# Kernel tuning notes

Hardware: AMD Instinct MI355X
Metric: run time of the kernel (lower is better)

The kernel has to match this reference:

```python
import jax, jax.numpy as jnp
import numpy as np

EPS = 1e-12  # torch F.normalize eps
NUM_HEADS = 4
DT = 0.25
NUM_STEPS = 4


def _l2norm(x, axis=-1):
    n = jnp.sqrt(jnp.sum(x * x, axis=axis, keepdims=True))
    return x / jnp.maximum(n, EPS)


def setup_inputs() -> dict:
    key = jax.random.key(0)
    k0, k1, k2, k3, k4 = jax.random.split(key, 5)
    B, T, D = 4, 2048, 256
    z = jax.random.normal(k0, (B, T, D), dtype=jnp.float32)
    omega = jax.random.normal(k1, (1, 1, D), dtype=jnp.float32) * 0.1
    Wqk = jax.random.normal(k2, (2 * D, D), dtype=jnp.float32) * (1.0 / np.sqrt(D))
    Wout = jax.random.normal(k3, (D, D), dtype=jnp.float32) * (1.0 / np.sqrt(D))
    bout = jax.random.normal(k4, (D,), dtype=jnp.float32) * 0.01
    return {"z": z, "omega": omega, "Wqk": Wqk, "Wout": Wout, "bout": bout}


def _kuramoto(x, omega, Wqk, Wout, bout):
    # x: [B, T, D]
    B, T, D = x.shape
    hd = D // NUM_HEADS
    qk = x @ Wqk.T  # [B, T, 2D]
    q, k = jnp.split(qk, 2, axis=-1)
    q = _l2norm(q.reshape(B, T, NUM_HEADS, hd))  # cosine-normalized per head
    k = _l2norm(k.reshape(B, T, NUM_HEADS, hd))
    # coupling: [B, H, T, T] cosine similarity
    coupling = jnp.einsum("bqhd,bkhd->bhqk", q, k)
    # sin nonlinearity replaces softmax
    force = jnp.einsum("bhqk,bkhd->bqhd", jnp.sin(coupling), k).reshape(B, T, D)
    return omega + force @ Wout.T + bout


def reference(z, omega, Wqk, Wout, bout):
    def f(x):
        return _kuramoto(x, omega, Wqk, Wout, bout)

    x = z
    for _ in range(NUM_STEPS):
        x = _l2norm(x)
        k1 = f(x)
        k2 = f(x + DT / 2 * k1)
        k3 = f(x + DT / 2 * k2)
        k4 = f(x + DT * k3)
        x = x + DT / 6 * (k1 + 2 * k2 + 2 * k3 + k4)
    return _l2norm(x)
```

## Files before the change

kernel.cpp:

```cpp
#include <hip/hip_runtime.h>
#include <cmath>

#define NB 4
#define TT 2048
#define DD 256
#define NH 4
#define BT (NB*TT)

static constexpr float DT_ = 0.25f;

typedef _Float16 f16x8 __attribute__((ext_vector_type(8)));
typedef _Float16 f16x4 __attribute__((ext_vector_type(4)));
typedef float    f32x4 __attribute__((ext_vector_type(4)));

static constexpr size_t HSZ = (size_t)NB * NH * TT * 64;
static constexpr size_t FSZ = (size_t)BT * 256;

__device__ __forceinline__ void gload16(const void* g, void* l) {
    __builtin_amdgcn_global_load_lds(
        (const __attribute__((address_space(1))) void*)g,
        (__attribute__((address_space(3))) void*)l,
        16, 0, 0);
}

__global__ __launch_bounds__(256)
void split_weights(const float* __restrict__ Wqk, const float* __restrict__ Wout,
                   _Float16* __restrict__ WqkH, _Float16* __restrict__ WqkL,
                   _Float16* __restrict__ WoutH, _Float16* __restrict__ WoutL)
{
    const int idx = blockIdx.x * 256 + threadIdx.x;
    const float4 v = (idx < 32768) ? ((const float4*)Wqk)[idx]
                                   : ((const float4*)Wout)[idx - 32768];
    f16x4 h, l;
    h[0]=(_Float16)v.x; l[0]=(_Float16)(v.x-(float)h[0]);
    h[1]=(_Float16)v.y; l[1]=(_Float16)(v.y-(float)h[1]);
    h[2]=(_Float16)v.z; l[2]=(_Float16)(v.z-(float)h[2]);
    h[3]=(_Float16)v.w; l[3]=(_Float16)(v.w-(float)h[3]);
    if (idx < 32768) { ((f16x4*)WqkH)[idx] = h; ((f16x4*)WqkL)[idx] = l; }
    else { ((f16x4*)WoutH)[idx-32768] = h; ((f16x4*)WoutL)[idx-32768] = l; }
}

__global__ __launch_bounds__(256)
void comb_weights(const float* __restrict__ Wqk, const float* __restrict__ Wout,
                  const float* __restrict__ omega, const float* __restrict__ bout,
                  _Float16* __restrict__ WcombH, _Float16* __restrict__ WcombL,
                  float* __restrict__ qkob)
{
    __shared__ float qrow[256];
    __shared__ float pr[256];
    const int n = blockIdx.x;
    const int k = threadIdx.x;
    qrow[k] = Wqk[n * 256 + k];
    __syncthreads();
    float s = 0.f;
    for (int m = 0; m < 256; ++m) s = fmaf(qrow[m], Wout[m * 256 + k], s);
    const _Float16 h = (_Float16)s;
    WcombH[n * 256 + k] = h;
    WcombL[n * 256 + k] = (_Float16)(s - (float)h);
    pr[k] = (omega[k] + bout[k]) * qrow[k];
    __syncthreads();
    if (k == 0) {
        float t = 0.f;
        for (int i = 0; i < 256; ++i) t += pr[i];
        qkob[n] = t;
    }
}

__global__ __launch_bounds__(256)
void l2norm_rows(const float* __restrict__ src, float* __restrict__ dst,
                 _Float16* __restrict__ dstH, _Float16* __restrict__ dstL) {
    const int wave = threadIdx.x >> 6;
    const int lane = threadIdx.x & 63;
    const size_t row = (size_t)blockIdx.x * 4 + wave;
    float4 v = ((const float4*)(src + row * DD))[lane];
    float ss = v.x*v.x + v.y*v.y + v.z*v.z + v.w*v.w;
    #pragma unroll
    for (int off = 32; off; off >>= 1) ss += __shfl_xor(ss, off, 64);
    const float inv = 1.0f / fmaxf(sqrtf(ss), 1e-12f);
    v.x *= inv; v.y *= inv; v.z *= inv; v.w *= inv;
    ((float4*)(dst + row * DD))[lane] = v;
    if (dstH != nullptr) {
        f16x4 h, l;
        h[0]=(_Float16)v.x; l[0]=(_Float16)(v.x-(float)h[0]);
        h[1]=(_Float16)v.y; l[1]=(_Float16)(v.y-(float)h[1]);
        h[2]=(_Float16)v.z; l[2]=(_Float16)(v.z-(float)h[2]);
        h[3]=(_Float16)v.w; l[3]=(_Float16)(v.w-(float)h[3]);
        ((f16x4*)(dstH + row * DD))[lane] = h;
        ((f16x4*)(dstL + row * DD))[lane] = l;
    }
}

__global__ __launch_bounds__(256)
void reduce_F(const float* __restrict__ Fp, float* __restrict__ Facc,
              _Float16* __restrict__ SH, _Float16* __restrict__ SL, int faccm)
{
    const size_t idx = (size_t)blockIdx.x * 256 + threadIdx.x;
    const float4 a = ((const float4*)Fp)[idx];
    const float4 b = ((const float4*)(Fp + FSZ))[idx];
    const float4 c = ((const float4*)(Fp + 2*FSZ))[idx];
    float4 s = make_float4(a.x+b.x+c.x, a.y+b.y+c.y, a.z+b.z+c.z, a.w+b.w+c.w);
    if (faccm == 1) {
        ((float4*)Facc)[idx] = s;
    } else if (faccm == 2) {
        float4 f = ((const float4*)Facc)[idx];
        f.x += 2.f*s.x; f.y += 2.f*s.y; f.z += 2.f*s.z; f.w += 2.f*s.w;
        ((float4*)Facc)[idx] = f;
    } else {
        const float4 f = ((const float4*)Facc)[idx];
        s.x += f.x; s.y += f.y; s.z += f.z; s.w += f.w;
    }
    f16x4 h, l;
    h[0]=(_Float16)s.x; l[0]=(_Float16)(s.x-(float)h[0]);
    h[1]=(_Float16)s.y; l[1]=(_Float16)(s.y-(float)h[1]);
    h[2]=(_Float16)s.z; l[2]=(_Float16)(s.z-(float)h[2]);
    h[3]=(_Float16)s.w; l[3]=(_Float16)(s.w-(float)h[3]);
    ((f16x4*)SH)[idx] = h;
    ((f16x4*)SL)[idx] = l;
}

__global__ __launch_bounds__(256, 3)
void gemm_mfma(const _Float16* __restrict__ AH, const _Float16* __restrict__ AL,
               const _Float16* __restrict__ BH, const _Float16* __restrict__ BL,
               float* __restrict__ qkx, const float* __restrict__ qkob,
               const float* __restrict__ omega, const float* __restrict__ bout,
               const float* __restrict__ xin, float* __restrict__ xout,
               _Float16* __restrict__ Qhi, _Float16* __restrict__ Qlo,
               _Float16* __restrict__ Khi, _Float16* __restrict__ Klo,
               _Float16* __restrict__ KtrH,
               int mode, float cc)
{
    __shared__ _Float16 Ah[128 * 64];
    __shared__ _Float16 Al[128 * 64];
    __shared__ _Float16 Bh[64 * 64];
    __shared__ _Float16 Bl[64 * 64];
    const int m0 = blockIdx.x * 128, n0 = blockIdx.y * 64;
    const int t  = threadIdx.x;
    const int w  = t >> 6;
    const int l  = t & 63;
    const int lr = l & 15;
    const int lq = l >> 4;
    const int m7 = lr & 7;
    const int rr = l >> 3;
    const int cg = ((l & 7) ^ rr) * 8;

    f32x4 acc[2][4];
    #pragma unroll
    for (int s = 0; s < 2; ++s)
        #pragma unroll
        for (int nt = 0; nt < 4; ++nt) acc[s][nt] = (f32x4){0.f,0.f,0.f,0.f};

    for (int kc = 0; kc < 4; ++kc) {
        const int k0 = kc * 64;
        __syncthreads();
        #pragma unroll
        for (int a = 0; a < 4; ++a) {
            const int rg = 8*w + 32*a;
            gload16(AH + (size_t)(m0 + rg + rr) * 256 + k0 + cg, &Ah[rg * 64]);
            gload16(AL + (size_t)(m0 + rg + rr) * 256 + k0 + cg, &Al[rg * 64]);
            if (a < 2) {
                gload16(BH + (size_t)(n0 + rg + rr) * 256 + k0 + cg, &Bh[rg * 64]);
                gload16(BL + (size_t)(n0 + rg + rr) * 256 + k0 + cg, &Bl[rg * 64]);
            }
        }
        __syncthreads();
        #pragma unroll
        for (int c = 0; c < 2; ++c) {
            const int xo = (((4*c + lq) ^ m7) << 4);
            f16x8 ah[2], al[2], bh[4], bl[4];
            #pragma unroll
            for (int s = 0; s < 2; ++s) {
                ah[s] = *(const f16x8*)((const char*)Ah + (32*w + 16*s + lr) * 128 + xo);
                al[s] = *(const f16x8*)((const char*)Al + (32*w + 16*s + lr) * 128 + xo);
            }
            #pragma unroll
            for (int nt = 0; nt < 4; ++nt) {
                bh[nt] = *(const f16x8*)((const char*)Bh + (16*nt + lr) * 128 + xo);
                bl[nt] = *(const f16x8*)((const char*)Bl + (16*nt + lr) * 128 + xo);
            }
            #pragma unroll
            for (int s = 0; s < 2; ++s)
                #pragma unroll
                for (int nt = 0; nt < 4; ++nt) {
                    acc[s][nt] = __builtin_amdgcn_mfma_f32_16x16x32_f16(ah[s], bh[nt], acc[s][nt], 0, 0, 0);
                    acc[s][nt] = __builtin_amdgcn_mfma_f32_16x16x32_f16(ah[s], bl[nt], acc[s][nt], 0, 0, 0);
                    acc[s][nt] = __builtin_amdgcn_mfma_f32_16x16x32_f16(al[s], bh[nt], acc[s][nt], 0, 0, 0);
                }
        }
    }

    if (mode == 2) {
        #pragma unroll
        for (int s = 0; s < 2; ++s) {
            const int row0 = m0 + 32*w + 16*s + 4*lq;
            #pragma unroll
            for (int nt = 0; nt < 4; ++nt) {
                const int col = n0 + 16*nt + lr;
                const float ob = omega[col] + bout[col];
                #pragma unroll
                for (int r = 0; r < 4; ++r) {
                    const size_t off = (size_t)(row0 + r) * 256 + col;
                    xout[off] = xin[off] + (DT_ / 6.0f) * acc[s][nt][r] + DT_ * ob;
                }
            }
        }
    } else {
        float val[2][4][4];
        #pragma unroll
        for (int s = 0; s < 2; ++s) {
            const int row0 = m0 + 32*w + 16*s + 4*lq;
            #pragma unroll
            for (int nt = 0; nt < 4; ++nt) {
                const int col = n0 + 16*nt + lr;
                #pragma unroll
                for (int r = 0; r < 4; ++r) {
                    const size_t qo = (size_t)(row0 + r) * 512 + col;
                    if (mode == 0) {
                        val[s][nt][r] = acc[s][nt][r];
                        qkx[qo] = acc[s][nt][r];
                    } else {
                        val[s][nt][r] = qkx[qo] + cc * (acc[s][nt][r] + qkob[col]);
                    }
                }
            }
        }
        float ss[2][4];
        #pragma unroll
        for (int s = 0; s < 2; ++s)
            #pragma unroll
            for (int r = 0; r < 4; ++r) {
                float v = 0.f;
                #pragma unroll
                for (int nt = 0; nt < 4; ++nt) v += val[s][nt][r] * val[s][nt][r];
                ss[s][r] = v;
            }
        #pragma unroll
        for (int off = 1; off < 16; off <<= 1)
            #pragma unroll
            for (int s = 0; s < 2; ++s)
                #pragma unroll
                for (int r = 0; r < 4; ++r)
                    ss[s][r] += __shfl_xor(ss[s][r], off, 64);
        const int  b    = m0 >> 11;
        const int  h    = (n0 >> 6) & 3;
        const bool is_k = (n0 >= 256);
        const size_t bhi = (size_t)b * NH + h;
        _Float16* dhi = (is_k ? Khi : Qhi) + bhi * (size_t)TT * 64;
        _Float16* dlo = (is_k ? Klo : Qlo) + bhi * (size_t)TT * 64;
        const int mloc = m0 & (TT - 1);
        #pragma unroll
        for (int s = 0; s < 2; ++s) {
            const int r0 = 32*w + 16*s + 4*lq;
            float inv[4];
            #pragma unroll
            for (int r = 0; r < 4; ++r) inv[r] = 1.0f / fmaxf(sqrtf(ss[s][r]), 1e-12f);
            #pragma unroll
            for (int nt = 0; nt < 4; ++nt) {
                const int d = 16*nt + lr;
                f16x4 hv, lv;
                #pragma unroll
                for (int r = 0; r < 4; ++r) {
                    const float v2 = val[s][nt][r] * inv[r];
                    hv[r] = (_Float16)v2;
                    lv[r] = (_Float16)(v2 - (float)hv[r]);
                    dhi[(size_t)(mloc + r0 + r) * 64 + d] = hv[r];
                    dlo[(size_t)(mloc + r0 + r) * 64 + d] = lv[r];
                }
                if (is_k) {
                    const size_t tb = bhi * (size_t)64 * TT + (size_t)d * TT + mloc + r0;
                    *(f16x4*)(KtrH + tb) = hv;
                }
            }
        }
    }
}

__global__ __launch_bounds__(256, 3)
void kuramoto_attn(const _Float16* __restrict__ Qhi, const _Float16* __restrict__ Qlo,
                   const _Float16* __restrict__ Khi, const _Float16* __restrict__ Klo,
                   const _Float16* __restrict__ KtrH,
                   float* __restrict__ Fp)
{
    __shared__ _Float16 KjH[64 * 64];
    __shared__ _Float16 KjL[64 * 64];
    __shared__ _Float16 KdH[64 * 64];
    __shared__ _Float16 Pw[4][2][16 * 64];
    const int bh = blockIdx.x;
    const int b  = bh >> 2, h = bh & 3;
    const size_t base  = (size_t)bh * TT * 64;
    const size_t tbase = (size_t)bh * 64 * TT;
    const int t0 = blockIdx.y * 11;
    const int tn = (blockIdx.y == 2) ? 10 : 11;
    float* Fout = Fp + (size_t)blockIdx.y * FSZ;
    const int t = threadIdx.x;
    const int w = t >> 6;
    const int l = t & 63;
    const int lr = l & 15;
    const int lq = l >> 4;
    const int i0 = blockIdx.z * 128 + w * 32;
    const int m7 = lr & 7;
    const int x0 = ((lq ^ m7) << 4);
    const int x1 = (((lq + 4) ^ m7) << 4);
    const int rr = l >> 3;
    const int lc8 = (l & 7) * 8;
    const int sw = ((l & 7) ^ rr) * 8;
    const int rg = 8 * w + rr;

    f16x8 qh[2][2], ql[2][2];
    #pragma unroll
    for (int s = 0; s < 2; ++s) {
        const size_t qoff = base + (size_t)(i0 + 16*s + lr) * 64 + lq * 8;
        qh[s][0] = *(const f16x8*)(Qhi + qoff);
        qh[s][1] = *(const f16x8*)(Qhi + qoff + 32);
        ql[s][0] = *(const f16x8*)(Qlo + qoff);
        ql[s][1] = *(const f16x8*)(Qlo + qoff + 32);
    }

    f32x4 Facc[2][4];
    #pragma unroll
    for (int s = 0; s < 2; ++s)
        #pragma unroll
        for (int nt = 0; nt < 4; ++nt) Facc[s][nt] = (f32x4){0.f, 0.f, 0.f, 0.f};

    uint4 gA0, gA1, gB0, gB1, gC0, gC1;
#define GLOAD(TTi) do { \
        const int j0_ = (t0 + (TTi)) * 64; \
        gA0 = *(const uint4*)(Khi  + base  + (size_t)(j0_ + rg)      * 64 + lc8); \
        gA1 = *(const uint4*)(Khi  + base  + (size_t)(j0_ + rg + 32) * 64 + lc8); \
        gB0 = *(const uint4*)(Klo  + base  + (size_t)(j0_ + rg)      * 64 + lc8); \
        gB1 = *(const uint4*)(Klo  + base  + (size_t)(j0_ + rg + 32) * 64 + lc8); \
        gC0 = *(const uint4*)(KtrH + tbase + (size_t)rg        * TT + j0_ + lc8); \
        gC1 = *(const uint4*)(KtrH + tbase + (size_t)(rg + 32) * TT + j0_ + lc8); \
    } while (0)

    GLOAD(0);

    for (int tt = 0; tt < tn; ++tt) {
        *(uint4*)&KjH[rg * 64 + sw]        = gA0;
        *(uint4*)&KjH[(rg + 32) * 64 + sw] = gA1;
        *(uint4*)&KjL[rg * 64 + sw]        = gB0;
        *(uint4*)&KjL[(rg + 32) * 64 + sw] = gB1;
        *(uint4*)&KdH[rg * 64 + sw]        = gC0;
        *(uint4*)&KdH[(rg + 32) * 64 + sw] = gC1;
        if (tt + 1 < tn) GLOAD(tt + 1);
        asm volatile("s_waitcnt lgkmcnt(0)" ::: "memory");
        __builtin_amdgcn_s_barrier();
        asm volatile("" ::: "memory");

        #pragma unroll
        for (int nt = 0; nt < 4; ++nt) {
            const int rb = (16*nt + lr) * 128;
            f16x8 kh0 = *(const f16x8*)((const char*)KjH + rb + x0);
            f16x8 kh1 = *(const f16x8*)((const char*)KjH + rb + x1);
            f16x8 kl0 = *(const f16x8*)((const char*)KjL + rb + x0);
            f16x8 kl1 = *(const f16x8*)((const char*)KjL + rb + x1);
            #pragma unroll
            for (int s = 0; s < 2; ++s) {
                f32x4 a = (f32x4){0.f, 0.f, 0.f, 0.f};
                __builtin_amdgcn_s_setprio(1);
                a = __builtin_amdgcn_mfma_f32_16x16x32_f16(kh0, qh[s][0], a, 0, 0, 0);
                a = __builtin_amdgcn_mfma_f32_16x16x32_f16(kh1, qh[s][1], a, 0, 0, 0);
                a = __builtin_amdgcn_mfma_f32_16x16x32_f16(kl0, qh[s][0], a, 0, 0, 0);
                a = __builtin_amdgcn_mfma_f32_16x16x32_f16(kl1, qh[s][1], a, 0, 0, 0);
                a = __builtin_amdgcn_mfma_f32_16x16x32_f16(kh0, ql[s][0], a, 0, 0, 0);
                a = __builtin_amdgcn_mfma_f32_16x16x32_f16(kh1, ql[s][1], a, 0, 0, 0);
                __builtin_amdgcn_s_setprio(0);
                f16x4 pv;
                #pragma unroll
                for (int r = 0; r < 4; ++r) pv[r] = (_Float16)__sinf(a[r]);
                *(f16x4*)((char*)&Pw[w][0][0] + ((int)sizeof(_Float16))*0 + s * 2048 + lr * 128
                          + (((2*nt + (lq >> 1)) ^ m7) << 4) + ((lq & 1) << 3)) = pv;
            }
        }
        f16x8 ph[2][2];
        #pragma unroll
        for (int s = 0; s < 2; ++s) {
            ph[s][0] = *(const f16x8*)((const char*)&Pw[w][0][0] + s * 2048 + lr * 128 + x0);
            ph[s][1] = *(const f16x8*)((const char*)&Pw[w][0][0] + s * 2048 + lr * 128 + x1);
        }
        #pragma unroll
        for (int nt = 0; nt < 4; ++nt) {
            const int rb = (16*nt + lr) * 128;
            f16x8 kh0 = *(const f16x8*)((const char*)KdH + rb + x0);
            f16x8 kh1 = *(const f16x8*)((const char*)KdH + rb + x1);
            __builtin_amdgcn_s_setprio(1);
            #pragma unroll
            for (int s = 0; s < 2; ++s) {
                Facc[s][nt] = __builtin_amdgcn_mfma_f32_16x16x32_f16(ph[s][0], kh0, Facc[s][nt], 0, 0, 0);
                Facc[s][nt] = __builtin_amdgcn_mfma_f32_16x16x32_f16(ph[s][1], kh1, Facc[s][nt], 0, 0, 0);
            }
            __builtin_amdgcn_s_setprio(0);
        }
        __builtin_amdgcn_s_barrier();
        asm volatile("" ::: "memory");
    }
#undef GLOAD

    #pragma unroll
    for (int s = 0; s < 2; ++s) {
        float* fo = Fout + ((size_t)b * TT + i0 + 16*s + 4*lq) * 256 + h * 64 + lr;
        #pragma unroll
        for (int nt = 0; nt < 4; ++nt)
            #pragma unroll
            for (int r = 0; r < 4; ++r)
                fo[(size_t)r * 256 + nt * 16] = Facc[s][nt][r];
    }
}

extern "C" void kernel_launch(void* const* d_in, const int* in_sizes, int n_in,
                              void* d_out, int out_size, void* d_ws, size_t ws_size,
                              hipStream_t stream) {
    const float* z     = (const float*)d_in[0];
    const float* omega = (const float*)d_in[1];
    const float* Wqk   = (const float*)d_in[2];
    const float* Wout  = (const float*)d_in[3];
    const float* bout  = (const float*)d_in[4];

    float* x    = (float*)d_ws;
    float* Facc = x + FSZ;
    float* Fp   = Facc + FSZ;
    float* qkx  = Fp + 3 * FSZ;
    float* qkob = qkx + (size_t)BT * 512;
    _Float16* xsH  = (_Float16*)(qkob + 512);
    _Float16* xsL  = xsH  + FSZ;
    _Float16* Qhi  = xsL  + FSZ;
    _Float16* Qlo  = Qhi  + HSZ;
    _Float16* Khi  = Qlo  + HSZ;
    _Float16* Klo  = Khi  + HSZ;
    _Float16* KtrH = Klo  + HSZ;
    _Float16* WqkH = KtrH + HSZ;
    _Float16* WqkL = WqkH + (size_t)512 * 256;
    _Float16* WoutH= WqkL + (size_t)512 * 256;
    _Float16* WoutL= WoutH + (size_t)256 * 256;
    _Float16* WcombH = WoutL + (size_t)256 * 256;
    _Float16* WcombL = WcombH + (size_t)512 * 256;

    split_weights<<<192, 256, 0, stream>>>(Wqk, Wout, WqkH, WqkL, WoutH, WoutL);
    comb_weights<<<512, 256, 0, stream>>>(Wqk, Wout, omega, bout, WcombH, WcombL, qkob);

    for (int step = 0; step < 4; ++step) {
        l2norm_rows<<<BT / 4, 256, 0, stream>>>(step == 0 ? z : x, x, xsH, xsL);
        gemm_mfma<<<dim3(BT / 128, 8), 256, 0, stream>>>(
            xsH, xsL, WqkH, WqkL, qkx, nullptr,
            nullptr, nullptr, nullptr, nullptr,
            Qhi, Qlo, Khi, Klo, KtrH, 0, 0.f);
        kuramoto_attn<<<dim3(NB * NH, 3, TT / 128), 256, 0, stream>>>(
            Qhi, Qlo, Khi, Klo, KtrH, Fp);
        for (int s = 1; s <= 3; ++s) {
            const float cs = (s == 3) ? 0.25f : 0.125f;
            reduce_F<<<2048, 256, 0, stream>>>(Fp, Facc, xsH, xsL, (s == 1) ? 1 : 2);
            gemm_mfma<<<dim3(BT / 128, 8), 256, 0, stream>>>(
                xsH, xsL, WcombH, WcombL, qkx, qkob,
                nullptr, nullptr, nullptr, nullptr,
                Qhi, Qlo, Khi, Klo, KtrH, 1, cs);
            kuramoto_attn<<<dim3(NB * NH, 3, TT / 128), 256, 0, stream>>>(
                Qhi, Qlo, Khi, Klo, KtrH, Fp);
        }
        reduce_F<<<2048, 256, 0, stream>>>(Fp, Facc, xsH, xsL, 3);
        gemm_mfma<<<dim3(BT / 128, 4), 256, 0, stream>>>(
            xsH, xsL, WoutH, WoutL, nullptr, nullptr,
            omega, bout, x, x,
            nullptr, nullptr, nullptr, nullptr, nullptr, 2, 0.f);
    }
    l2norm_rows<<<BT / 4, 256, 0, stream>>>(x, (float*)d_out, nullptr, nullptr);
}
```

Baseline: 1.161 ms.

## Prefetch next K-chunk in GEMM and stage transposed K through LDS

The GEMM main loop now loads all fragments of a chunk into registers, then issues the global-to-LDS loads for the next chunk before running the MFMAs, so memory traffic overlaps with compute. Launch bounds drop from 3 to 2 waves per SIMD to allow the extra fragment registers. The transposed K output is first written to a swizzled LDS tile and then stored with coalesced 16-byte global writes instead of scattered 8-byte writes. The trade-off is lower occupancy and an extra barrier in the K epilogue.

Result: no change. 1.153 ms, median of 2 (-0.6%).

```diff
diff --git a/kernel.cpp b/kernel.cpp
--- a/kernel.cpp
+++ b/kernel.cpp
@@ -118,7 +118,7 @@
     ((f16x4*)SL)[idx] = l;
 }
 
-__global__ __launch_bounds__(256, 3)
+__global__ __launch_bounds__(256, 2)
 void gemm_mfma(const _Float16* __restrict__ AH, const _Float16* __restrict__ AL,
                const _Float16* __restrict__ BH, const _Float16* __restrict__ BL,
                float* __restrict__ qkx, const float* __restrict__ qkob,
@@ -149,44 +149,57 @@
         #pragma unroll
         for (int nt = 0; nt < 4; ++nt) acc[s][nt] = (f32x4){0.f,0.f,0.f,0.f};
 
+#define GSTAGE(K0) do { \
+        _Pragma("unroll") \
+        for (int a = 0; a < 4; ++a) { \
+            const int rg = 8*w + 32*a; \
+            gload16(AH + (size_t)(m0 + rg + rr) * 256 + (K0) + cg, &Ah[rg * 64]); \
+            gload16(AL + (size_t)(m0 + rg + rr) * 256 + (K0) + cg, &Al[rg * 64]); \
+            if (a < 2) { \
+                gload16(BH + (size_t)(n0 + rg + rr) * 256 + (K0) + cg, &Bh[rg * 64]); \
+                gload16(BL + (size_t)(n0 + rg + rr) * 256 + (K0) + cg, &Bl[rg * 64]); \
+            } \
+        } \
+    } while (0)
+
+    GSTAGE(0);
+    asm volatile("s_waitcnt vmcnt(0)" ::: "memory");
+    __builtin_amdgcn_s_barrier();
+
     for (int kc = 0; kc < 4; ++kc) {
-        const int k0 = kc * 64;
-        __syncthreads();
-        #pragma unroll
-        for (int a = 0; a < 4; ++a) {
-            const int rg = 8*w + 32*a;
-            gload16(AH + (size_t)(m0 + rg + rr) * 256 + k0 + cg, &Ah[rg * 64]);
-            gload16(AL + (size_t)(m0 + rg + rr) * 256 + k0 + cg, &Al[rg * 64]);
-            if (a < 2) {
-                gload16(BH + (size_t)(n0 + rg + rr) * 256 + k0 + cg, &Bh[rg * 64]);
-                gload16(BL + (size_t)(n0 + rg + rr) * 256 + k0 + cg, &Bl[rg * 64]);
-            }
-        }
-        __syncthreads();
+        f16x8 ah[2][2], al[2][2], bh[2][4], bl[2][4];
         #pragma unroll
         for (int c = 0; c < 2; ++c) {
             const int xo = (((4*c + lq) ^ m7) << 4);
-            f16x8 ah[2], al[2], bh[4], bl[4];
             #pragma unroll
             for (int s = 0; s < 2; ++s) {
-                ah[s] = *(const f16x8*)((const char*)Ah + (32*w + 16*s + lr) * 128 + xo);
-                al[s] = *(const f16x8*)((const char*)Al + (32*w + 16*s + lr) * 128 + xo);
+                ah[c][s] = *(const f16x8*)((const char*)Ah + (32*w + 16*s + lr) * 128 + xo);
+                al[c][s] = *(const f16x8*)((const char*)Al + (32*w + 16*s + lr) * 128 + xo);
             }
             #pragma unroll
             for (int nt = 0; nt < 4; ++nt) {
-                bh[nt] = *(const f16x8*)((const char*)Bh + (16*nt + lr) * 128 + xo);
-                bl[nt] = *(const f16x8*)((const char*)Bl + (16*nt + lr) * 128 + xo);
-            }
+                bh[c][nt] = *(const f16x8*)((const char*)Bh + (16*nt + lr) * 128 + xo);
+                bl[c][nt] = *(const f16x8*)((const char*)Bl + (16*nt + lr) * 128 + xo);
+            }
+        }
+        asm volatile("s_waitcnt lgkmcnt(0)" ::: "memory");
+        __builtin_amdgcn_s_barrier();
+        if (kc < 3) GSTAGE((kc + 1) * 64);
+        #pragma unroll
+        for (int c = 0; c < 2; ++c)
             #pragma unroll
             for (int s = 0; s < 2; ++s)
                 #pragma unroll
                 for (int nt = 0; nt < 4; ++nt) {
-                    acc[s][nt] = __builtin_amdgcn_mfma_f32_16x16x32_f16(ah[s], bh[nt], acc[s][nt], 0, 0, 0);
-                    acc[s][nt] = __builtin_amdgcn_mfma_f32_16x16x32_f16(ah[s], bl[nt], acc[s][nt], 0, 0, 0);
-                    acc[s][nt] = __builtin_amdgcn_mfma_f32_16x16x32_f16(al[s], bh[nt], acc[s][nt], 0, 0, 0);
+                    acc[s][nt] = __builtin_amdgcn_mfma_f32_16x16x32_f16(ah[c][s], bh[c][nt], acc[s][nt], 0, 0, 0);
+                    acc[s][nt] = __builtin_amdgcn_mfma_f32_16x16x32_f16(ah[c][s], bl[c][nt], acc[s][nt], 0, 0, 0);
+                    acc[s][nt] = __builtin_amdgcn_mfma_f32_16x16x32_f16(al[c][s], bh[c][nt], acc[s][nt], 0, 0, 0);
                 }
-        }
-    }
+        if (kc < 3) asm volatile("s_waitcnt vmcnt(0)" ::: "memory");
+        __builtin_amdgcn_s_barrier();
+        asm volatile("" ::: "memory");
+    }
+#undef GSTAGE
 
     if (mode == 2) {
         #pragma unroll
@@ -247,6 +260,7 @@
         _Float16* dhi = (is_k ? Khi : Qhi) + bhi * (size_t)TT * 64;
         _Float16* dlo = (is_k ? Klo : Qlo) + bhi * (size_t)TT * 64;
         const int mloc = m0 & (TT - 1);
+        _Float16* Pt = Ah;
         #pragma unroll
         for (int s = 0; s < 2; ++s) {
             const int r0 = 32*w + 16*s + 4*lq;
@@ -266,9 +280,19 @@
                     dlo[(size_t)(mloc + r0 + r) * 64 + d] = lv[r];
                 }
                 if (is_k) {
-                    const size_t tb = bhi * (size_t)64 * TT + (size_t)d * TT + mloc + r0;
-                    *(f16x4*)(KtrH + tb) = hv;
+                    *(f16x4*)((char*)Pt + d * 256 + ((r0 * 2) ^ ((d & 7) << 4))) = hv;
                 }
+            }
+        }
+        if (is_k) {
+            __syncthreads();
+            const size_t kb = bhi * (size_t)64 * TT + mloc;
+            #pragma unroll
+            for (int p = 0; p < 4; ++p) {
+                const int d   = (t >> 4) + 16 * p;
+                const int lm0 = (t & 15) * 8;
+                f16x8 v = *(const f16x8*)((const char*)Pt + d * 256 + ((lm0 * 2) ^ ((d & 7) << 4)));
+                *(f16x8*)(KtrH + kb + (size_t)d * TT + lm0) = v;
             }
         }
     }
@@ -367,7 +391,7 @@
                 f16x4 pv;
                 #pragma unroll
                 for (int r = 0; r < 4; ++r) pv[r] = (_Float16)__sinf(a[r]);
-                *(f16x4*)((char*)&Pw[w][0][0] + ((int)sizeof(_Float16))*0 + s * 2048 + lr * 128
+                *(f16x4*)((char*)&Pw[w][0][0] + s * 2048 + lr * 128
                           + (((2*nt + (lq >> 1)) ^ m7) << 4) + ((lq & 1) << 3)) = pv;
             }
         }
```
